# Performance work log

Measured on AMD Instinct MI355X. Metric: run time of the kernel, lower is better.

Reference implementation:

```python
import jax, jax.numpy as jnp
import numpy as np

N, E, G, D, H, EMB, L = 200000, 3200000, 4096, 64, 64, 128, 3


def setup_inputs() -> dict:
    key = jax.random.key(0)
    ks = jax.random.split(key, 16)
    s = 0.05
    inp = {}
    inp["x_a"] = jax.random.normal(ks[0], (N, D), jnp.float32)
    inp["edge_index"] = jax.random.randint(ks[1], (2, E), 0, N)
    inp["batch"] = jnp.sort(jax.random.randint(ks[2], (N,), 0, G))
    inp["acid_idx"] = jax.random.randint(ks[3], (G,), 0, 2)
    inp["concentration"] = jax.random.uniform(ks[4], (G,), jnp.float32)
    inp["num_graphs"] = G
    # GIN MLP params per layer (input_dim_a == hl_size == 64, so stackable)
    inp["W1s"] = jax.random.normal(ks[5], (L, D, H), jnp.float32) * s
    inp["b1s"] = jnp.zeros((L, H), jnp.float32)
    inp["gammas"] = jnp.ones((L, H), jnp.float32)
    inp["betas"] = jnp.zeros((L, H), jnp.float32)
    inp["bn_means"] = jnp.zeros((L, H), jnp.float32)   # eval-mode running stats
    inp["bn_vars"] = jnp.ones((L, H), jnp.float32)
    inp["W2s"] = jax.random.normal(ks[6], (L, H, H), jnp.float32) * s
    inp["b2s"] = jnp.zeros((L, H), jnp.float32)
    inp["emb_acid"] = jax.random.normal(ks[7], (2, EMB), jnp.float32)
    inp["emb_conc"] = jax.random.normal(ks[8], (2, EMB), jnp.float32)
    FC_IN = H * L + 2 * EMB  # 448
    inp["fc1_W"] = jax.random.normal(ks[9], (FC_IN, H), jnp.float32) * s
    inp["fc1_b"] = jnp.zeros((H,), jnp.float32)
    inp["fc2_W"] = jax.random.normal(ks[10], (H, 2), jnp.float32) * s
    inp["fc2_b"] = jnp.zeros((2,), jnp.float32)
    return inp


def reference(x_a, edge_index, batch, acid_idx, concentration, num_graphs,
              W1s, b1s, gammas, betas, bn_means, bn_vars, W2s, b2s,
              emb_acid, emb_conc, fc1_W, fc1_b, fc2_W, fc2_b):
    src, dst = edge_index[0], edge_index[1]
    n_nodes = x_a.shape[0]
    x = x_a
    pooled = []
    for l in range(W1s.shape[0]):  # structurally distinct layers (params differ)
        # GINConv, eps=0: MLP(x + sum_{j->i} x_j)
        agg = jax.ops.segment_sum(x[src], dst, num_segments=n_nodes)
        h = x + agg
        h = h @ W1s[l] + b1s[l]
        # BatchNorm1d in eval mode (running stats)
        h = (h - bn_means[l]) * jax.lax.rsqrt(bn_vars[l] + 1e-5) * gammas[l] + betas[l]
        h = jax.nn.relu(h)
        h = jax.nn.relu(h @ W2s[l] + b2s[l])
        x = h  # dropout inactive at eval
        pooled.append(jax.ops.segment_sum(x, batch, num_segments=num_graphs))
    xg = jnp.concatenate(pooled, axis=1)  # [G, L*H]
    conc_idx = jnp.where(concentration == 0.5, 0, 1)
    feat = jnp.concatenate([xg, emb_acid[acid_idx], emb_conc[conc_idx]], axis=1)
    h = jax.nn.relu(feat @ fc1_W + fc1_b)  # dropout inactive at eval
    out = jax.nn.sigmoid(h @ fc2_W + fc2_b)
    return out
```

## Files before the change

### kernel.cpp

```cpp
#include <hip/hip_runtime.h>
#include <math.h>


static __device__ __forceinline__ float rlf(float v, int k) {
    return __int_as_float(__builtin_amdgcn_readlane(__float_as_int(v), k));
}
static __device__ __forceinline__ int rli(int v, int k) {
    return __builtin_amdgcn_readlane(v, k);
}


__global__ void k_hist(const int* __restrict__ dst, int* __restrict__ deg, int E) {
    int i = blockIdx.x * blockDim.x + threadIdx.x;
    int stride = gridDim.x * blockDim.x;
    for (; i < E; i += stride) atomicAdd(&deg[dst[i]], 1);
}

#define SCAN_B 512

__global__ void k_scan1(const int* __restrict__ deg, int* __restrict__ ex,
                        int* __restrict__ bsum, int n) {
    __shared__ int s[SCAN_B];
    int t = threadIdx.x;
    int i = blockIdx.x * SCAN_B + t;
    int v = (i < n) ? deg[i] : 0;
    s[t] = v;
    __syncthreads();
    for (int off = 1; off < SCAN_B; off <<= 1) {
        int tv = (t >= off) ? s[t - off] : 0;
        __syncthreads();
        s[t] += tv;
        __syncthreads();
    }
    if (i < n) ex[i] = s[t] - v;
    if (t == SCAN_B - 1) bsum[blockIdx.x] = s[t];
}

__global__ void k_scan2(int* __restrict__ bsum, int nb) {
    __shared__ int s[SCAN_B];
    int t = threadIdx.x;
    int v = (t < nb) ? bsum[t] : 0;
    s[t] = v;
    __syncthreads();
    for (int off = 1; off < SCAN_B; off <<= 1) {
        int tv = (t >= off) ? s[t - off] : 0;
        __syncthreads();
        s[t] += tv;
        __syncthreads();
    }
    if (t < nb) bsum[t] = s[t] - v;
}

__global__ void k_scan3(int* __restrict__ ex, const int* __restrict__ bsum,
                        int n, int E) {
    int i = blockIdx.x * SCAN_B + threadIdx.x;
    if (i < n) ex[i] += bsum[blockIdx.x];
    if (blockIdx.x == 0 && threadIdx.x == 0) ex[n] = E;
}

__global__ void k_scatter(const int* __restrict__ src, const int* __restrict__ dst,
                          const int* __restrict__ row_start, int* __restrict__ cur,
                          int* __restrict__ csr, int E) {
    int i = blockIdx.x * blockDim.x + threadIdx.x;
    int stride = gridDim.x * blockDim.x;
    for (; i < E; i += stride) {
        int d = dst[i];
        int p = atomicAdd(&cur[d], 1);
        csr[row_start[d] + p] = src[i];
    }
}

__global__ void k_gstart(const int* __restrict__ batch, int* __restrict__ gs,
                         int n, int G) {
    int g = blockIdx.x * blockDim.x + threadIdx.x;
    if (g > G) return;
    if (g == G) { gs[G] = n; return; }
    int lo = 0, hi = n;
    while (lo < hi) {
        int mid = (lo + hi) >> 1;
        if (batch[mid] < g) lo = mid + 1; else hi = mid;
    }
    gs[g] = lo;
}

__global__ void k_wt(const float* __restrict__ W, float* __restrict__ Wt, int total) {
    int i = blockIdx.x * blockDim.x + threadIdx.x;
    if (i >= total) return;
    int l = i >> 12, r = i & 4095, j = r >> 6, k = r & 63;
    Wt[(l << 12) + (j << 6) + k] = W[(l << 12) + (k << 6) + j];
}


__global__ __launch_bounds__(256) void k_gather(
    const float* __restrict__ x, const int* __restrict__ row_start,
    const int* __restrict__ csr, float* __restrict__ agg, int n)
{
    int lane = threadIdx.x & 63;
    int wid = (blockIdx.x * blockDim.x + threadIdx.x) >> 6;
    int nw = (gridDim.x * blockDim.x) >> 6;
    for (int node = wid; node < n; node += nw) {
        float acc = x[(size_t)node * 64 + lane];
        int s0 = row_start[node], s1 = row_start[node + 1];
        int j = s0;
        for (; j + 16 <= s1; j += 16) {
            int idx = csr[j + (lane & 15)];
            float a[16];
#pragma unroll
            for (int u = 0; u < 16; ++u)
                a[u] = x[(size_t)rli(idx, u) * 64 + lane];
            float t0 = (a[0] + a[1]) + (a[2] + a[3]);
            float t1 = (a[4] + a[5]) + (a[6] + a[7]);
            float t2 = (a[8] + a[9]) + (a[10] + a[11]);
            float t3 = (a[12] + a[13]) + (a[14] + a[15]);
            acc += (t0 + t1) + (t2 + t3);
        }
        int cnt = s1 - j;
        if (cnt) {
            int idx = csr[j + (lane & 15)];
            float s = 0.f;
#pragma unroll
            for (int u = 0; u < 16; ++u) {
                int jc = (u < cnt) ? u : 0;
                float a = x[(size_t)rli(idx, jc) * 64 + lane];
                s += (u < cnt) ? a : 0.f;
            }
            acc += s;
        }
        agg[(size_t)node * 64 + lane] = acc;
    }
}


__global__ __launch_bounds__(256, 2) void k_gemm(
    float* __restrict__ xb,
    const float* __restrict__ Wt1, const float* __restrict__ b1,
    const float* __restrict__ gamma, const float* __restrict__ beta,
    const float* __restrict__ mean, const float* __restrict__ var,
    const float* __restrict__ Wt2, const float* __restrict__ b2, int n)
{
    int lane = threadIdx.x & 63;
    int wid = (blockIdx.x * blockDim.x + threadIdx.x) >> 6;
    int nw = (gridDim.x * blockDim.x) >> 6;

    float4 w1v[16], w2v[16];
    const float4* W1p = (const float4*)Wt1 + (size_t)lane * 16;
    const float4* W2p = (const float4*)Wt2 + (size_t)lane * 16;
#pragma unroll
    for (int q = 0; q < 16; ++q) w1v[q] = W1p[q];
#pragma unroll
    for (int q = 0; q < 16; ++q) w2v[q] = W2p[q];
#pragma unroll
    for (int q = 0; q < 16; ++q) {
        asm volatile("" : "+v"(w1v[q].x), "+v"(w1v[q].y), "+v"(w1v[q].z), "+v"(w1v[q].w));
        asm volatile("" : "+v"(w2v[q].x), "+v"(w2v[q].y), "+v"(w2v[q].z), "+v"(w2v[q].w));
    }

    float bias1 = b1[lane];
    float sc = gamma[lane] * rsqrtf(var[lane] + 1e-5f);
    float sh = beta[lane] - mean[lane] * sc;
    float bias2 = b2[lane];

    int node = wid;
    float a = (node < n) ? xb[(size_t)node * 64 + lane] : 0.f;
    while (node < n) {
        int nxt = node + nw;
        float anx = (nxt < n) ? xb[(size_t)nxt * 64 + lane] : 0.f;

        float h0 = bias1, h1 = 0.f, h2 = 0.f, h3 = 0.f;
#pragma unroll
        for (int q = 0; q < 16; ++q) {
            h0 += rlf(a, 4 * q + 0) * w1v[q].x;
            h1 += rlf(a, 4 * q + 1) * w1v[q].y;
            h2 += rlf(a, 4 * q + 2) * w1v[q].z;
            h3 += rlf(a, 4 * q + 3) * w1v[q].w;
        }
        float h = fmaxf(((h0 + h1) + (h2 + h3)) * sc + sh, 0.f);

        float o0 = bias2, o1 = 0.f, o2 = 0.f, o3 = 0.f;
#pragma unroll
        for (int q = 0; q < 16; ++q) {
            o0 += rlf(h, 4 * q + 0) * w2v[q].x;
            o1 += rlf(h, 4 * q + 1) * w2v[q].y;
            o2 += rlf(h, 4 * q + 2) * w2v[q].z;
            o3 += rlf(h, 4 * q + 3) * w2v[q].w;
        }
        xb[(size_t)node * 64 + lane] = fmaxf((o0 + o1) + (o2 + o3), 0.f);

        node = nxt;
        a = anx;
    }
}


__global__ __launch_bounds__(256) void k_pool(const float* __restrict__ x,
                                              const int* __restrict__ gs,
                                              float* __restrict__ pooled,
                                              int G, int l, int lh) {
    int lane = threadIdx.x & 63;
    int wid = (blockIdx.x * blockDim.x + threadIdx.x) >> 6;
    if (wid >= G) return;
    int s0 = gs[wid], s1 = gs[wid + 1];
    float a0 = 0, a1 = 0, a2 = 0, a3 = 0;
    int nd = s0;
    for (; nd + 4 <= s1; nd += 4) {
        a0 += x[(size_t)(nd + 0) * 64 + lane];
        a1 += x[(size_t)(nd + 1) * 64 + lane];
        a2 += x[(size_t)(nd + 2) * 64 + lane];
        a3 += x[(size_t)(nd + 3) * 64 + lane];
    }
    for (; nd < s1; ++nd) a0 += x[(size_t)nd * 64 + lane];
    pooled[(size_t)wid * lh + l * 64 + lane] = (a0 + a1) + (a2 + a3);
}


__global__ __launch_bounds__(256) void k_fc(
    const float* __restrict__ pooled, const int* __restrict__ acid,
    const float* __restrict__ conc, const float* __restrict__ emb_acid,
    const float* __restrict__ emb_conc, const float* __restrict__ fc1W,
    const float* __restrict__ fc1b, const float* __restrict__ fc2W,
    const float* __restrict__ fc2b, float* __restrict__ out, int G, int lh)
{
    __shared__ float sf[4][448];
    int lane = threadIdx.x & 63;
    int w = threadIdx.x >> 6;
    int g = blockIdx.x * 4 + w;
    int fcin = lh + 256;
    if (g < G) {
        const float* pr = pooled + (size_t)g * lh;
        for (int c = lane; c < lh; c += 64) sf[w][c] = pr[c];
        const float* ea = emb_acid + acid[g] * 128;
        int ci = (conc[g] == 0.5f) ? 0 : 1;
        const float* ec = emb_conc + ci * 128;
        sf[w][lh + lane] = ea[lane];
        sf[w][lh + 64 + lane] = ea[lane + 64];
        sf[w][lh + 128 + lane] = ec[lane];
        sf[w][lh + 192 + lane] = ec[lane + 64];
    }
    __syncthreads();
    if (g >= G) return;
    float h0 = fc1b[lane], h1 = 0.f;
    for (int k = 0; k + 2 <= fcin; k += 2) {
        h0 += sf[w][k] * fc1W[(size_t)k * 64 + lane];
        h1 += sf[w][k + 1] * fc1W[(size_t)(k + 1) * 64 + lane];
    }
    float h = fmaxf(h0 + h1, 0.f);
    float p0 = h * fc2W[lane * 2 + 0];
    float p1 = h * fc2W[lane * 2 + 1];
    for (int off = 32; off; off >>= 1) {
        p0 += __shfl_xor(p0, off, 64);
        p1 += __shfl_xor(p1, off, 64);
    }
    if (lane == 0) {
        out[g * 2 + 0] = 1.0f / (1.0f + expf(-(p0 + fc2b[0])));
        out[g * 2 + 1] = 1.0f / (1.0f + expf(-(p1 + fc2b[1])));
    }
}


extern "C" void kernel_launch(void* const* d_in, const int* in_sizes, int n_in,
                              void* d_out, int out_size, void* d_ws, size_t ws_size,
                              hipStream_t stream)
{
    const float* x_a      = (const float*)d_in[0];
    const int*   ei       = (const int*)d_in[1];
    const int*   batch    = (const int*)d_in[2];
    const int*   acid     = (const int*)d_in[3];
    const float* conc     = (const float*)d_in[4];
    const float* W1s      = (const float*)d_in[6];
    const float* b1s      = (const float*)d_in[7];
    const float* gammas   = (const float*)d_in[8];
    const float* betas    = (const float*)d_in[9];
    const float* bn_means = (const float*)d_in[10];
    const float* bn_vars  = (const float*)d_in[11];
    const float* W2s      = (const float*)d_in[12];
    const float* b2s      = (const float*)d_in[13];
    const float* emb_acid = (const float*)d_in[14];
    const float* emb_conc = (const float*)d_in[15];
    const float* fc1W     = (const float*)d_in[16];
    const float* fc1b     = (const float*)d_in[17];
    const float* fc2W     = (const float*)d_in[18];
    const float* fc2b     = (const float*)d_in[19];

    const int N = in_sizes[0] / 64;
    const int E = in_sizes[1] / 2;
    const int G = in_sizes[3];
    const int L = in_sizes[6] / (64 * 64);
    const int LH = 64 * L;

    char* ws = (char*)d_ws;
    size_t off = 0;
    auto alloc = [&](size_t bytes) -> void* {
        void* p = ws + off;
        off += (bytes + 255) & ~(size_t)255;
        return p;
    };
    float* buf0      = (float*)alloc((size_t)N * 64 * 4);
    float* buf1      = (float*)alloc((size_t)N * 64 * 4);
    float* pooled    = (float*)alloc((size_t)G * LH * 4);
    int*   row_start = (int*)alloc((size_t)(N + 1) * 4);
    int*   deg       = (int*)alloc((size_t)N * 4);
    int*   csr       = (int*)alloc((size_t)E * 4);
    int*   bsum      = (int*)alloc(4096);
    int*   gs        = (int*)alloc((size_t)(G + 1) * 4);
    float* Wt1       = (float*)alloc((size_t)L * 4096 * 4);
    float* Wt2       = (float*)alloc((size_t)L * 4096 * 4);

    const int* srcv = ei;
    const int* dstv = ei + E;

    hipMemsetAsync(deg, 0, (size_t)N * 4, stream);
    k_hist<<<4096, 256, 0, stream>>>(dstv, deg, E);
    int nb = (N + SCAN_B - 1) / SCAN_B;
    k_scan1<<<nb, SCAN_B, 0, stream>>>(deg, row_start, bsum, N);
    k_scan2<<<1, SCAN_B, 0, stream>>>(bsum, nb);
    k_scan3<<<nb, SCAN_B, 0, stream>>>(row_start, bsum, N, E);
    hipMemsetAsync(deg, 0, (size_t)N * 4, stream);
    k_scatter<<<4096, 256, 0, stream>>>(srcv, dstv, row_start, deg, csr, E);
    k_gstart<<<(G + 256) / 256, 256, 0, stream>>>(batch, gs, N, G);

    int wtot = L * 4096;
    k_wt<<<(wtot + 255) / 256, 256, 0, stream>>>(W1s, Wt1, wtot);
    k_wt<<<(wtot + 255) / 256, 256, 0, stream>>>(W2s, Wt2, wtot);

    const float* xin = x_a;
    float* bufs[2] = {buf0, buf1};
    for (int l = 0; l < L; ++l) {
        float* xb = bufs[l & 1];
        k_gather<<<4096, 256, 0, stream>>>(xin, row_start, csr, xb, N);
        k_gemm<<<2048, 256, 0, stream>>>(
            xb, Wt1 + (size_t)l * 4096, b1s + l * 64,
            gammas + l * 64, betas + l * 64,
            bn_means + l * 64, bn_vars + l * 64,
            Wt2 + (size_t)l * 4096, b2s + l * 64, N);
        k_pool<<<(G + 3) / 4, 256, 0, stream>>>(xb, gs, pooled, G, l, LH);
        xin = xb;
    }

    k_fc<<<(G + 3) / 4, 256, 0, stream>>>(pooled, acid, conc, emb_acid, emb_conc,
                                          fc1W, fc1b, fc2W, fc2b,
                                          (float*)d_out, G, LH);
}
```

Before: 1.201 ms.

## Vectorize neighbor gather with float4 lanes and fuse GIN MLP with graph pooling

```diff
diff --git a/kernel.cpp b/kernel.cpp
--- a/kernel.cpp
+++ b/kernel.cpp
@@ -4,9 +4,6 @@
 
 static __device__ __forceinline__ float rlf(float v, int k) {
     return __int_as_float(__builtin_amdgcn_readlane(__float_as_int(v), k));
-}
-static __device__ __forceinline__ int rli(int v, int k) {
-    return __builtin_amdgcn_readlane(v, k);
 }
 
 
@@ -91,56 +88,74 @@
 }
 
 
-__global__ __launch_bounds__(256) void k_gather(
+__global__ __launch_bounds__(256, 4) void k_gather(
     const float* __restrict__ x, const int* __restrict__ row_start,
     const int* __restrict__ csr, float* __restrict__ agg, int n)
 {
     int lane = threadIdx.x & 63;
+    int g = lane >> 4;
+    int c16 = lane & 15;
     int wid = (blockIdx.x * blockDim.x + threadIdx.x) >> 6;
     int nw = (gridDim.x * blockDim.x) >> 6;
+
     for (int node = wid; node < n; node += nw) {
-        float acc = x[(size_t)node * 64 + lane];
         int s0 = row_start[node], s1 = row_start[node + 1];
+        float4 x4 = *(const float4*)&x[(size_t)node * 64 + c16 * 4];
+        float4 acc;
+        acc.x = g == 0 ? x4.x : 0.f;
+        acc.y = g == 0 ? x4.y : 0.f;
+        acc.z = g == 0 ? x4.z : 0.f;
+        acc.w = g == 0 ? x4.w : 0.f;
+
         int j = s0;
         for (; j + 16 <= s1; j += 16) {
-            int idx = csr[j + (lane & 15)];
-            float a[16];
-#pragma unroll
-            for (int u = 0; u < 16; ++u)
-                a[u] = x[(size_t)rli(idx, u) * 64 + lane];
-            float t0 = (a[0] + a[1]) + (a[2] + a[3]);
-            float t1 = (a[4] + a[5]) + (a[6] + a[7]);
-            float t2 = (a[8] + a[9]) + (a[10] + a[11]);
-            float t3 = (a[12] + a[13]) + (a[14] + a[15]);
-            acc += (t0 + t1) + (t2 + t3);
+            int i0 = csr[j + g + 0];
+            int i1 = csr[j + g + 4];
+            int i2 = csr[j + g + 8];
+            int i3 = csr[j + g + 12];
+            float4 a0 = *(const float4*)&x[(size_t)i0 * 64 + c16 * 4];
+            float4 a1 = *(const float4*)&x[(size_t)i1 * 64 + c16 * 4];
+            float4 a2 = *(const float4*)&x[(size_t)i2 * 64 + c16 * 4];
+            float4 a3 = *(const float4*)&x[(size_t)i3 * 64 + c16 * 4];
+            acc.x += (a0.x + a1.x) + (a2.x + a3.x);
+            acc.y += (a0.y + a1.y) + (a2.y + a3.y);
+            acc.z += (a0.z + a1.z) + (a2.z + a3.z);
+            acc.w += (a0.w + a1.w) + (a2.w + a3.w);
         }
         int cnt = s1 - j;
         if (cnt) {
-            int idx = csr[j + (lane & 15)];
-            float s = 0.f;
-#pragma unroll
-            for (int u = 0; u < 16; ++u) {
-                int jc = (u < cnt) ? u : 0;
-                float a = x[(size_t)rli(idx, jc) * 64 + lane];
-                s += (u < cnt) ? a : 0.f;
+#pragma unroll
+            for (int u = 0; u < 4; ++u) {
+                int p = g + 4 * u;
+                int idx = csr[j + (p < cnt ? p : 0)];
+                float4 a = *(const float4*)&x[(size_t)idx * 64 + c16 * 4];
+                if (p < cnt) {
+                    acc.x += a.x; acc.y += a.y; acc.z += a.z; acc.w += a.w;
+                }
             }
-            acc += s;
         }
-        agg[(size_t)node * 64 + lane] = acc;
-    }
-}
-
-
-__global__ __launch_bounds__(256, 2) void k_gemm(
+        acc.x += __shfl_xor(acc.x, 16); acc.y += __shfl_xor(acc.y, 16);
+        acc.z += __shfl_xor(acc.z, 16); acc.w += __shfl_xor(acc.w, 16);
+        acc.x += __shfl_xor(acc.x, 32); acc.y += __shfl_xor(acc.y, 32);
+        acc.z += __shfl_xor(acc.z, 32); acc.w += __shfl_xor(acc.w, 32);
+        if (lane < 16)
+            *(float4*)&agg[(size_t)node * 64 + c16 * 4] = acc;
+    }
+}
+
+
+__global__ __launch_bounds__(256, 2) void k_gemm_pool(
     float* __restrict__ xb,
+    const int* __restrict__ gs,
     const float* __restrict__ Wt1, const float* __restrict__ b1,
     const float* __restrict__ gamma, const float* __restrict__ beta,
     const float* __restrict__ mean, const float* __restrict__ var,
-    const float* __restrict__ Wt2, const float* __restrict__ b2, int n)
+    const float* __restrict__ Wt2, const float* __restrict__ b2,
+    float* __restrict__ pooled, int G, int lay, int lh)
 {
     int lane = threadIdx.x & 63;
     int wid = (blockIdx.x * blockDim.x + threadIdx.x) >> 6;
-    int nw = (gridDim.x * blockDim.x) >> 6;
+    if (wid >= G) return;
 
     float4 w1v[16], w2v[16];
     const float4* W1p = (const float4*)Wt1 + (size_t)lane * 16;
@@ -160,56 +175,40 @@
     float sh = beta[lane] - mean[lane] * sc;
     float bias2 = b2[lane];
 
-    int node = wid;
-    float a = (node < n) ? xb[(size_t)node * 64 + lane] : 0.f;
-    while (node < n) {
-        int nxt = node + nw;
-        float anx = (nxt < n) ? xb[(size_t)nxt * 64 + lane] : 0.f;
-
-        float h0 = bias1, h1 = 0.f, h2 = 0.f, h3 = 0.f;
-#pragma unroll
-        for (int q = 0; q < 16; ++q) {
-            h0 += rlf(a, 4 * q + 0) * w1v[q].x;
-            h1 += rlf(a, 4 * q + 1) * w1v[q].y;
-            h2 += rlf(a, 4 * q + 2) * w1v[q].z;
-            h3 += rlf(a, 4 * q + 3) * w1v[q].w;
+    int s0 = gs[wid], s1 = gs[wid + 1];
+    int g4 = lane >> 4, c16 = lane & 15;
+    float pacc = 0.f;
+
+    for (int nb = s0; nb < s1; nb += 4) {
+        int rowc = nb + g4; if (rowc > s1 - 1) rowc = s1 - 1;
+        float4 a4 = *(const float4*)&xb[(size_t)rowc * 64 + c16 * 4];
+
+#pragma unroll
+        for (int r = 0; r < 4; ++r) {
+            if (nb + r >= s1) break;
+            float h0 = bias1, h1 = 0.f, h2 = 0.f, h3 = 0.f;
+#pragma unroll
+            for (int q = 0; q < 16; ++q) {
+                h0 += rlf(a4.x, r * 16 + q) * w1v[q].x;
+                h1 += rlf(a4.y, r * 16 + q) * w1v[q].y;
+                h2 += rlf(a4.z, r * 16 + q) * w1v[q].z;
+                h3 += rlf(a4.w, r * 16 + q) * w1v[q].w;
+            }
+            float h = fmaxf(((h0 + h1) + (h2 + h3)) * sc + sh, 0.f);
+            float o0 = bias2, o1 = 0.f, o2 = 0.f, o3 = 0.f;
+#pragma unroll
+            for (int q = 0; q < 16; ++q) {
+                o0 += rlf(h, 4 * q + 0) * w2v[q].x;
+                o1 += rlf(h, 4 * q + 1) * w2v[q].y;
+                o2 += rlf(h, 4 * q + 2) * w2v[q].z;
+                o3 += rlf(h, 4 * q + 3) * w2v[q].w;
+            }
+            float o = fmaxf((o0 + o1) + (o2 + o3), 0.f);
+            xb[(size_t)(nb + r) * 64 + lane] = o;
+            pacc += o;
         }
-        float h = fmaxf(((h0 + h1) + (h2 + h3)) * sc + sh, 0.f);
-
-        float o0 = bias2, o1 = 0.f, o2 = 0.f, o3 = 0.f;
-#pragma unroll
-        for (int q = 0; q < 16; ++q) {
-            o0 += rlf(h, 4 * q + 0) * w2v[q].x;
-            o1 += rlf(h, 4 * q + 1) * w2v[q].y;
-            o2 += rlf(h, 4 * q + 2) * w2v[q].z;
-            o3 += rlf(h, 4 * q + 3) * w2v[q].w;
-        }
-        xb[(size_t)node * 64 + lane] = fmaxf((o0 + o1) + (o2 + o3), 0.f);
-
-        node = nxt;
-        a = anx;
-    }
-}
-
-
-__global__ __launch_bounds__(256) void k_pool(const float* __restrict__ x,
-                                              const int* __restrict__ gs,
-                                              float* __restrict__ pooled,
-                                              int G, int l, int lh) {
-    int lane = threadIdx.x & 63;
-    int wid = (blockIdx.x * blockDim.x + threadIdx.x) >> 6;
-    if (wid >= G) return;
-    int s0 = gs[wid], s1 = gs[wid + 1];
-    float a0 = 0, a1 = 0, a2 = 0, a3 = 0;
-    int nd = s0;
-    for (; nd + 4 <= s1; nd += 4) {
-        a0 += x[(size_t)(nd + 0) * 64 + lane];
-        a1 += x[(size_t)(nd + 1) * 64 + lane];
-        a2 += x[(size_t)(nd + 2) * 64 + lane];
-        a3 += x[(size_t)(nd + 3) * 64 + lane];
-    }
-    for (; nd < s1; ++nd) a0 += x[(size_t)nd * 64 + lane];
-    pooled[(size_t)wid * lh + l * 64 + lane] = (a0 + a1) + (a2 + a3);
+    }
+    pooled[(size_t)wid * lh + lay * 64 + lane] = pacc;
 }
 
 
@@ -294,8 +293,8 @@
         off += (bytes + 255) & ~(size_t)255;
         return p;
     };
-    float* buf0      = (float*)alloc((size_t)N * 64 * 4);
-    float* buf1      = (float*)alloc((size_t)N * 64 * 4);
+    float* buf0      = (float*)alloc(((size_t)N + 8) * 64 * 4);
+    float* buf1      = (float*)alloc(((size_t)N + 8) * 64 * 4);
     float* pooled    = (float*)alloc((size_t)G * LH * 4);
     int*   row_start = (int*)alloc((size_t)(N + 1) * 4);
     int*   deg       = (int*)alloc((size_t)N * 4);
@@ -327,12 +326,13 @@
     for (int l = 0; l < L; ++l) {
         float* xb = bufs[l & 1];
         k_gather<<<4096, 256, 0, stream>>>(xin, row_start, csr, xb, N);
-        k_gemm<<<2048, 256, 0, stream>>>(
-            xb, Wt1 + (size_t)l * 4096, b1s + l * 64,
+        k_gemm_pool<<<(G + 3) / 4, 256, 0, stream>>>(
+            xb, gs,
+            Wt1 + (size_t)l * 4096, b1s + l * 64,
             gammas + l * 64, betas + l * 64,
             bn_means + l * 64, bn_vars + l * 64,
-            Wt2 + (size_t)l * 4096, b2s + l * 64, N);
-        k_pool<<<(G + 3) / 4, 256, 0, stream>>>(xb, gs, pooled, G, l, LH);
+            Wt2 + (size_t)l * 4096, b2s + l * 64,
+            pooled, G, l, LH);
         xin = xb;
     }
 
```

New measurement: 1.201 ms. No clear change (-0.0%).
